# Kernel optimization log

Hardware: AMD Instinct MI355X
Metric: run time of the kernel (lower is better)

Reference implementation:

```python
import jax, jax.numpy as jnp
import numpy as np

N, L, D = 8, 2048, 128


def setup_inputs() -> dict:
    key = jax.random.key(0)
    k1, k2, k3, k4 = jax.random.split(key, 4)
    x_t = jax.random.normal(k1, (N, L, D), jnp.float32)
    x_f = jax.random.normal(k2, (N, L, D), jnp.float32)
    W = jax.random.normal(k3, (D, D), jnp.float32) / np.sqrt(D)  # proj weight (torch Linear layout)
    b = jax.random.normal(k4, (D,), jnp.float32) * 0.02
    return {"x_t": x_t, "x_f": x_f, "W": W, "b": b}


def _col_score(a, c, scale):
    # softmax attention with zeroed diagonal, then column-sum -> [N, L]
    att = jnp.einsum('nld,nmd->nlm', a, c) * scale
    att = jax.nn.softmax(att, axis=-1)
    att = att * (1.0 - jnp.eye(att.shape[-1], dtype=att.dtype))
    return jnp.sum(att, axis=1)


def _mask(score, time):
    # score: [N, L]; k-th extreme threshold, k = L//2
    k = int(0.5 * score.shape[1])
    if time:
        vals, _ = jax.lax.top_k(score, k)          # k largest, descending
        theta = vals[:, -1:]                        # k-th largest
        return score > theta
    else:
        vals, _ = jax.lax.top_k(-score, k)          # k smallest
        theta = -vals[:, -1:]                       # k-th smallest
        return score <= theta


def reference(x_t, x_f, W, b):
    scale = 1.0 / np.sqrt(W.shape[0])
    pt = x_t @ W.T + b
    pf = x_f @ W.T + b
    score_t = _col_score(pt, pt, scale)
    score_f = _col_score(pf, pf, scale)
    score_tf = _col_score(pt, pf, scale)
    score_ft = _col_score(pf, pt, scale)
    mask_t = _mask(score_t, False)
    mask_f = _mask(score_f, False)
    mask_tf = _mask(score_tf, True)   # computed in original forward (unused in blend)
    mask_ft = _mask(score_ft, True)
    mask_t1 = (mask_t & ~mask_f)[:, :, None]   # [N, L, 1] broadcast over D
    mask_f1 = (mask_f & ~mask_t)[:, :, None]
    x_t1 = jnp.where(mask_t1, x_f, x_t)
    x_f1 = jnp.where(mask_f1, x_t, x_f)
    return (0.5 * (x_t1 + x_t), 0.5 * (x_f1 + x_f))
```

## Files before the change

kernel.cpp:

```cpp
#include <hip/hip_runtime.h>
#include <math.h>

#define LL 2048
#define DD 128
#define NS 16
#define SLAB (LL * DD)
#define SCALE 0.08838834764831845f

typedef __attribute__((ext_vector_type(8))) short short8v;
typedef __attribute__((ext_vector_type(4))) float float4v;

__device__ __forceinline__ unsigned int f2bf(float f) {
    unsigned int u = __float_as_uint(f);
    u += 0x7fffu + ((u >> 16) & 1u);
    return u >> 16;
}

__device__ __forceinline__ void strip_decode(int bx, int by, int& ib, int& ns) {
    const int lin = by * 16 + bx;
    const int xcd = lin & 7;
    const int w   = lin >> 3;
    ns = xcd + 8 * (w & 1);
    ib = w >> 1;
}

__device__ __forceinline__ void gl_lds16(const void* g, void* l) {
    __builtin_amdgcn_global_load_lds(
        (const __attribute__((address_space(1))) void*)g,
        (__attribute__((address_space(3))) void*)l, 16, 0, 0);
}

__device__ __forceinline__ void stage512(
    const unsigned short* __restrict__ gT, unsigned short* lbuf, int tid)
{
    const int row = tid >> 2;
    const int oc  = (tid & 3) ^ ((row >> 1) & 3);
    const int sb  = tid & ~63;
    gl_lds16(gT + (size_t)row * DD + oc * 8, lbuf + (size_t)sb * 8);
}

#define STAGE_HALF(DST, GH, GL, KC) do {                       \
    stage512((GH) + (KC) * 32,       (DST)[0], tid);           \
    stage512((GL) + (KC) * 32,       (DST)[1], tid);           \
    stage512((GH) + ((KC) + 1) * 32, (DST)[2], tid);           \
    stage512((GL) + ((KC) + 1) * 32, (DST)[3], tid); } while (0)

#define ZEROACC(ACC) do {                                      \
    _Pragma("unroll") for (int rt = 0; rt < 4; ++rt)           \
    _Pragma("unroll") for (int ct = 0; ct < 2; ++ct)           \
    _Pragma("unroll") for (int r = 0; r < 4; ++r) (ACC)[rt][ct][r] = 0.f; } while (0)

#define KC2(ACC, CB, KI, AKC) do {                                           \
    const unsigned short* BhP = (CB)[2 * (KI)];                              \
    const unsigned short* BlP = (CB)[2 * (KI) + 1];                          \
    short8v bh[2], bl[2], alv[4];                                            \
    _Pragma("unroll")                                                        \
    for (int ct = 0; ct < 2; ++ct) {                                         \
        const int r = wc * 32 + ct * 16 + l16;                               \
        const int off = r * 32 + ((quad ^ ((r >> 1) & 3)) << 3);             \
        bh[ct] = *(const short8v*)&BhP[off];                                 \
        bl[ct] = *(const short8v*)&BlP[off];                                 \
    }                                                                        \
    _Pragma("unroll")                                                        \
    for (int rt = 0; rt < 4; ++rt) {                                         \
        const int r = wr * 64 + rt * 16 + l16;                               \
        const int off = r * 32 + ((quad ^ ((r >> 1) & 3)) << 3);             \
        alv[rt] = *(const short8v*)&Alpan[AKC][off];                         \
    }                                                                        \
    __builtin_amdgcn_s_setprio(1);                                           \
    _Pragma("unroll")                                                        \
    for (int rt = 0; rt < 4; ++rt)                                           \
    _Pragma("unroll")                                                        \
    for (int ct = 0; ct < 2; ++ct) {                                         \
        (ACC)[rt][ct] = __builtin_amdgcn_mfma_f32_16x16x32_bf16(ah[AKC][rt], bh[ct], (ACC)[rt][ct], 0, 0, 0); \
        (ACC)[rt][ct] = __builtin_amdgcn_mfma_f32_16x16x32_bf16(ah[AKC][rt], bl[ct], (ACC)[rt][ct], 0, 0, 0); \
        (ACC)[rt][ct] = __builtin_amdgcn_mfma_f32_16x16x32_bf16(alv[rt],     bh[ct], (ACC)[rt][ct], 0, 0, 0); \
    }                                                                        \
    __builtin_amdgcn_s_setprio(0); } while (0)

#define EPI1(ACC) do {                                         \
    _Pragma("unroll") for (int rt = 0; rt < 4; ++rt)           \
    _Pragma("unroll") for (int rg = 0; rg < 4; ++rg) {         \
        float e0 = __expf((ACC)[rt][0][rg] * SCALE);           \
        float e1 = __expf((ACC)[rt][1][rg] * SCALE);           \
        z[rt][rg] += e0 + e1; } } while (0)

#define EPI2(ACC, JBV) do {                                    \
    float colp0 = 0.f, colp1 = 0.f;                            \
    const bool dgj = ((JBV) == ib);                            \
    _Pragma("unroll") for (int rt = 0; rt < 4; ++rt)           \
    _Pragma("unroll") for (int rg = 0; rg < 4; ++rg) {         \
        const int rl = wr * 64 + rt * 16 + quad * 4 + rg;      \
        float e0 = __expf((ACC)[rt][0][rg] * SCALE);           \
        float e1 = __expf((ACC)[rt][1][rg] * SCALE);           \
        bool s0 = dgj && (rl == wc * 32 + l16);                \
        bool s1 = dgj && (rl == wc * 32 + 16 + l16);           \
        colp0 += s0 ? 0.f : e0 * wrow[rt][rg];                 \
        colp1 += s1 ? 0.f : e1 * wrow[rt][rg]; }               \
    colp0 += __shfl_xor(colp0, 16); colp0 += __shfl_xor(colp0, 32); \
    colp1 += __shfl_xor(colp1, 16); colp1 += __shfl_xor(colp1, 32); \
    if (quad == 0) {                                           \
        scs[(JBV) * 128 + wc * 32 + l16][wr]      = colp0;     \
        scs[(JBV) * 128 + wc * 32 + 16 + l16][wr] = colp1; } } while (0)

__global__ __launch_bounds__(512) void proj_kernel(
    const float* __restrict__ xt, const float* __restrict__ xf,
    const float* __restrict__ W,  const float* __restrict__ bias,
    unsigned short* __restrict__ Ph, unsigned short* __restrict__ Pl)
{
    __shared__ float Wl[128 * 128];
    __shared__ float Xl[128 * 128];
    const int ns = blockIdx.y;
    const int l0 = blockIdx.x * 128;
    const int src = ns >> 3, n = ns & 7;
    const float* x = (src ? xf : xt) + (size_t)n * LL * DD + (size_t)l0 * DD;
    const int tid = threadIdx.x;
    const int ty = tid >> 4, tx = tid & 15;

#pragma unroll
    for (int it = 0; it < 8; ++it) {
        const int s   = it * 512 + tid;
        const int row = s >> 5, c = s & 31;
        const int oc  = c ^ (row & 7);
        const int sb  = it * 512 + (tid & ~63);
        gl_lds16(W + (size_t)row * DD + oc * 4, Wl + (size_t)sb * 4);
        gl_lds16(x + (size_t)row * DD + oc * 4, Xl + (size_t)sb * 4);
    }

    float acc[4][8];
#pragma unroll
    for (int i = 0; i < 4; ++i)
#pragma unroll
        for (int j = 0; j < 8; ++j) acc[i][j] = bias[tx + 16 * j];

    __syncthreads();

    const int rs = ty & 7, ds = tx & 7;
#pragma unroll 4
    for (int k4 = 0; k4 < 128; k4 += 4) {
        const int c = k4 >> 2;
        float4 xv[4], wv[8];
#pragma unroll
        for (int i = 0; i < 4; ++i)
            xv[i] = *(const float4*)&Xl[(ty + 32 * i) * 128 + ((c ^ rs) << 2)];
#pragma unroll
        for (int j = 0; j < 8; ++j)
            wv[j] = *(const float4*)&Wl[(tx + 16 * j) * 128 + ((c ^ ds) << 2)];
#pragma unroll
        for (int i = 0; i < 4; ++i)
#pragma unroll
            for (int j = 0; j < 8; ++j) {
                acc[i][j] = fmaf(xv[i].x, wv[j].x, acc[i][j]);
                acc[i][j] = fmaf(xv[i].y, wv[j].y, acc[i][j]);
                acc[i][j] = fmaf(xv[i].z, wv[j].z, acc[i][j]);
                acc[i][j] = fmaf(xv[i].w, wv[j].w, acc[i][j]);
            }
    }

#pragma unroll
    for (int i = 0; i < 4; ++i) {
        const size_t rowo = (size_t)ns * SLAB + (size_t)(l0 + ty + 32 * i) * DD;
#pragma unroll
        for (int j = 0; j < 8; ++j) {
            float p = acc[i][j];
            unsigned int hb = f2bf(p);
            float hf = __uint_as_float(hb << 16);
            unsigned int lb = f2bf(p - hf);
            Ph[rowo + tx + 16 * j] = (unsigned short)hb;
            Pl[rowo + tx + 16 * j] = (unsigned short)lb;
        }
    }
}

__global__ __launch_bounds__(512, 2) void score_kernel(
    const unsigned short* __restrict__ Ph, const unsigned short* __restrict__ Pl,
    float* __restrict__ Spart)
{
    __shared__ unsigned short pan[2][4][4096];
    __shared__ unsigned short Alpan[4][4096];
    __shared__ float scs[2048][2];
    __shared__ float zl[128][4];
    int ib, ns;  strip_decode(blockIdx.x, blockIdx.y, ib, ns);
    const int tid = threadIdx.x;
    const int lane = tid & 63, quad = lane >> 4, l16 = lane & 15, wave = tid >> 6;
    const int wr = wave >> 2, wc = wave & 3;

    const unsigned short* sAh = Ph + (size_t)ns * SLAB + (size_t)ib * 128 * DD;
    const unsigned short* sAl = Pl + (size_t)ns * SLAB + (size_t)ib * 128 * DD;
    const unsigned short* sBh = Ph + (size_t)ns * SLAB;
    const unsigned short* sBl = Pl + (size_t)ns * SLAB;

    stage512(sAl,      Alpan[0], tid);
    stage512(sAl + 32, Alpan[1], tid);
    stage512(sAl + 64, Alpan[2], tid);
    stage512(sAl + 96, Alpan[3], tid);
    STAGE_HALF(pan[0], sBh, sBl, 0);
    short8v ah[4][4];
#pragma unroll
    for (int kc = 0; kc < 4; ++kc)
#pragma unroll
        for (int rt = 0; rt < 4; ++rt)
            ah[kc][rt] = *(const short8v*)
                &sAh[(size_t)(wr * 64 + rt * 16 + l16) * DD + kc * 32 + quad * 8];
    __syncthreads();

    float4v accA[4][2], accB[4][2];
    float z[4][4];
#pragma unroll
    for (int rt = 0; rt < 4; ++rt)
#pragma unroll
        for (int rg = 0; rg < 4; ++rg) z[rt][rg] = 0.f;

#pragma unroll 1
    for (int jp = 0; jp < 8; ++jp) {
        const unsigned short* b0h = sBh + (size_t)(2 * jp) * 128 * DD;
        const unsigned short* b0l = sBl + (size_t)(2 * jp) * 128 * DD;
        const unsigned short* b1h = b0h + 128 * DD;
        const unsigned short* b1l = b0l + 128 * DD;
        const unsigned short* b2h = b1h + 128 * DD;
        const unsigned short* b2l = b1l + 128 * DD;

        ZEROACC(accA);
        STAGE_HALF(pan[1], b0h, b0l, 2);
        KC2(accA, pan[0], 0, 0);
        KC2(accA, pan[0], 1, 1);
        if (jp) EPI1(accB);
        __syncthreads();

        STAGE_HALF(pan[0], b1h, b1l, 0);
        KC2(accA, pan[1], 0, 2);
        KC2(accA, pan[1], 1, 3);
        __syncthreads();

        ZEROACC(accB);
        STAGE_HALF(pan[1], b1h, b1l, 2);
        KC2(accB, pan[0], 0, 0);
        KC2(accB, pan[0], 1, 1);
        EPI1(accA);
        __syncthreads();

        if (jp < 7) STAGE_HALF(pan[0], b2h, b2l, 0);
        KC2(accB, pan[1], 0, 2);
        KC2(accB, pan[1], 1, 3);
        __syncthreads();
    }
    EPI1(accB);

#pragma unroll
    for (int rt = 0; rt < 4; ++rt)
#pragma unroll
        for (int rg = 0; rg < 4; ++rg) {
            float s = z[rt][rg];
            s += __shfl_xor(s, 1);
            s += __shfl_xor(s, 2);
            s += __shfl_xor(s, 4);
            s += __shfl_xor(s, 8);
            if (l16 == 0) zl[wr * 64 + rt * 16 + quad * 4 + rg][wc] = s;
        }
    STAGE_HALF(pan[0], sBh, sBl, 0);
    __syncthreads();
    float wrow[4][4];
#pragma unroll
    for (int rt = 0; rt < 4; ++rt)
#pragma unroll
        for (int rg = 0; rg < 4; ++rg) {
            const int row = wr * 64 + rt * 16 + quad * 4 + rg;
            wrow[rt][rg] = 1.0f / (zl[row][0] + zl[row][1] + zl[row][2] + zl[row][3]);
        }

#pragma unroll 1
    for (int jp = 0; jp < 8; ++jp) {
        const unsigned short* b0h = sBh + (size_t)(2 * jp) * 128 * DD;
        const unsigned short* b0l = sBl + (size_t)(2 * jp) * 128 * DD;
        const unsigned short* b1h = b0h + 128 * DD;
        const unsigned short* b1l = b0l + 128 * DD;
        const unsigned short* b2h = b1h + 128 * DD;
        const unsigned short* b2l = b1l + 128 * DD;

        ZEROACC(accA);
        STAGE_HALF(pan[1], b0h, b0l, 2);
        KC2(accA, pan[0], 0, 0);
        KC2(accA, pan[0], 1, 1);
        if (jp) EPI2(accB, 2 * jp - 1);
        __syncthreads();

        STAGE_HALF(pan[0], b1h, b1l, 0);
        KC2(accA, pan[1], 0, 2);
        KC2(accA, pan[1], 1, 3);
        __syncthreads();

        ZEROACC(accB);
        STAGE_HALF(pan[1], b1h, b1l, 2);
        KC2(accB, pan[0], 0, 0);
        KC2(accB, pan[0], 1, 1);
        EPI2(accA, 2 * jp);
        __syncthreads();

        if (jp < 7) STAGE_HALF(pan[0], b2h, b2l, 0);
        KC2(accB, pan[1], 0, 2);
        KC2(accB, pan[1], 1, 3);
        __syncthreads();
    }
    EPI2(accB, 15);

    __syncthreads();
#pragma unroll
    for (int g = 0; g < 4; ++g) {
        const int m = tid + g * 512;
        Spart[((size_t)ns * LL + m) * 16 + ib] = scs[m][0] + scs[m][1];
    }
}

__global__ __launch_bounds__(512) void mask_kernel(
    const float* __restrict__ Spart, unsigned char* __restrict__ maskbuf)
{
    __shared__ double s[LL];
    __shared__ int cp[4][128];
    const int sl = blockIdx.x;
    const int ns = blockIdx.y;
    const int tid = threadIdx.x;
    const int r = tid & 127, g = tid >> 7;

#pragma unroll
    for (int q = 0; q < 4; ++q) {
        int m = tid + q * 512;
        const float* sp = Spart + ((size_t)ns * LL + m) * 16;
        double a = 0.0;
#pragma unroll
        for (int t = 0; t < 16; ++t) a += (double)sp[t];
        s[m] = a;
    }
    __syncthreads();

    const double si = s[sl * 128 + r];
    const double2* sv = (const double2*)s;
    const int base = g * 256;
    int cnt = 0;
#pragma unroll 8
    for (int j = 0; j < 256; ++j) {
        double2 p = sv[base + j];
        cnt += (p.x < si) ? 1 : 0;
        cnt += (p.y < si) ? 1 : 0;
    }
    cp[g][r] = cnt;
    __syncthreads();
    if (tid < 128) {
        int c = cp[0][tid] + cp[1][tid] + cp[2][tid] + cp[3][tid];
        maskbuf[ns * LL + sl * 128 + tid] = (c < 1024) ? 1 : 0;
    }
}

__global__ __launch_bounds__(256) void blend_kernel(
    const float* __restrict__ xt, const float* __restrict__ xf,
    const unsigned char* __restrict__ maskbuf, float* __restrict__ out)
{
    const int idx4 = blockIdx.x * 256 + threadIdx.x;
    const size_t q = (size_t)idx4 * 4;
    const int row = (int)(q >> 7);
    const float4 a = *(const float4*)(xt + q);
    const float4 b = *(const float4*)(xf + q);
    const int mt = maskbuf[row] & 1;
    const int mf = maskbuf[16384 + row] & 1;
    const bool ct = mt && !mf;
    const bool cf = mf && !mt;
    float4 av;
    av.x = 0.5f * (a.x + b.x);  av.y = 0.5f * (a.y + b.y);
    av.z = 0.5f * (a.z + b.z);  av.w = 0.5f * (a.w + b.w);
    float4 o0 = ct ? av : a;
    float4 o1 = cf ? av : b;
    *(float4*)(out + q)                   = o0;
    *(float4*)(out + (size_t)2097152 + q) = o1;
}

extern "C" void kernel_launch(void* const* d_in, const int* in_sizes, int n_in,
                              void* d_out, int out_size, void* d_ws, size_t ws_size,
                              hipStream_t stream)
{
    const float* xt = (const float*)d_in[0];
    const float* xf = (const float*)d_in[1];
    const float* W  = (const float*)d_in[2];
    const float* b  = (const float*)d_in[3];
    float* out = (float*)d_out;

    unsigned short* Ph = (unsigned short*)d_out;
    unsigned short* Pl = Ph + (size_t)NS * SLAB;

    float* Spart = (float*)d_ws;
    unsigned char* maskbuf = (unsigned char*)(Spart + (size_t)16 * LL * 16);

    proj_kernel<<<dim3(16, NS), 512, 0, stream>>>(xt, xf, W, b, Ph, Pl);
    score_kernel<<<dim3(16, 16), 512, 0, stream>>>(Ph, Pl, Spart);
    mask_kernel<<<dim3(16, NS), 512, 0, stream>>>(Spart, maskbuf);
    blend_kernel<<<2048, 256, 0, stream>>>(xt, xf, maskbuf, out);
}
```

Baseline: 197.4 us.

## Double-buffer K-chunks in projection kernel with 8x8 register tiles

Result: slower. 260.2 us (+31.8%).

```diff
diff --git a/kernel.cpp b/kernel.cpp
--- a/kernel.cpp
+++ b/kernel.cpp
@@ -103,71 +103,87 @@
         scs[(JBV) * 128 + wc * 32 + l16][wr]      = colp0;     \
         scs[(JBV) * 128 + wc * 32 + 16 + l16][wr] = colp1; } } while (0)
 
-__global__ __launch_bounds__(512) void proj_kernel(
+__global__ __launch_bounds__(256, 2) void proj_kernel(
     const float* __restrict__ xt, const float* __restrict__ xf,
     const float* __restrict__ W,  const float* __restrict__ bias,
     unsigned short* __restrict__ Ph, unsigned short* __restrict__ Pl)
 {
-    __shared__ float Wl[128 * 128];
-    __shared__ float Xl[128 * 128];
+    __shared__ float Xb[2][128 * 32];
+    __shared__ float Wb[2][128 * 32];
     const int ns = blockIdx.y;
     const int l0 = blockIdx.x * 128;
     const int src = ns >> 3, n = ns & 7;
     const float* x = (src ? xf : xt) + (size_t)n * LL * DD + (size_t)l0 * DD;
     const int tid = threadIdx.x;
-    const int ty = tid >> 4, tx = tid & 15;
-
-#pragma unroll
-    for (int it = 0; it < 8; ++it) {
-        const int s   = it * 512 + tid;
-        const int row = s >> 5, c = s & 31;
-        const int oc  = c ^ (row & 7);
-        const int sb  = it * 512 + (tid & ~63);
-        gl_lds16(W + (size_t)row * DD + oc * 4, Wl + (size_t)sb * 4);
-        gl_lds16(x + (size_t)row * DD + oc * 4, Xl + (size_t)sb * 4);
-    }
-
-    float acc[4][8];
-#pragma unroll
-    for (int i = 0; i < 4; ++i)
-#pragma unroll
-        for (int j = 0; j < 8; ++j) acc[i][j] = bias[tx + 16 * j];
-
-    __syncthreads();
-
-    const int rs = ty & 7, ds = tx & 7;
-#pragma unroll 4
-    for (int k4 = 0; k4 < 128; k4 += 4) {
-        const int c = k4 >> 2;
-        float4 xv[4], wv[8];
-#pragma unroll
-        for (int i = 0; i < 4; ++i)
-            xv[i] = *(const float4*)&Xl[(ty + 32 * i) * 128 + ((c ^ rs) << 2)];
-#pragma unroll
-        for (int j = 0; j < 8; ++j)
-            wv[j] = *(const float4*)&Wl[(tx + 16 * j) * 128 + ((c ^ ds) << 2)];
-#pragma unroll
-        for (int i = 0; i < 4; ++i)
+    const int tx = tid & 15, ty = tid >> 4;
+
+#define PSTAGE(BUF, G, KC) do {                                              \
+    _Pragma("unroll")                                                        \
+    for (int it = 0; it < 4; ++it) {                                         \
+        const int s   = it * 256 + tid;                                      \
+        const int sb  = it * 256 + (tid & ~63);                              \
+        const int row = s >> 3, cp = s & 7;                                  \
+        const int oc  = cp ^ (row & 7) ^ ((row >> 3) & 7);                   \
+        gl_lds16((G) + (size_t)row * DD + (KC) * 32 + oc * 4,                \
+                 (BUF) + (size_t)sb * 4);                                    \
+    } } while (0)
+
+    float acc[8][8];
+#pragma unroll
+    for (int i = 0; i < 8; ++i)
+#pragma unroll
+        for (int j = 0; j < 8; ++j) acc[i][j] = bias[tx * 8 + j];
+
+    PSTAGE(Xb[0], x, 0);
+    PSTAGE(Wb[0], W, 0);
+    __syncthreads();
+
+#pragma unroll
+    for (int kc = 0; kc < 4; ++kc) {
+        if (kc < 3) {
+            PSTAGE(Xb[(kc + 1) & 1], x, kc + 1);
+            PSTAGE(Wb[(kc + 1) & 1], W, kc + 1);
+        }
+        const float* Xc = Xb[kc & 1];
+        const float* Wc = Wb[kc & 1];
+#pragma unroll
+        for (int c = 0; c < 8; ++c) {
+            float4 xv[8], wv[8];
+#pragma unroll
+            for (int i = 0; i < 8; ++i) {
+                const int r = ty * 8 + i;
+                xv[i] = *(const float4*)&Xc[r * 32 + ((c ^ i ^ (ty & 7)) << 2)];
+            }
 #pragma unroll
             for (int j = 0; j < 8; ++j) {
-                acc[i][j] = fmaf(xv[i].x, wv[j].x, acc[i][j]);
-                acc[i][j] = fmaf(xv[i].y, wv[j].y, acc[i][j]);
-                acc[i][j] = fmaf(xv[i].z, wv[j].z, acc[i][j]);
-                acc[i][j] = fmaf(xv[i].w, wv[j].w, acc[i][j]);
+                const int r = tx * 8 + j;
+                wv[j] = *(const float4*)&Wc[r * 32 + ((c ^ j ^ (tx & 7)) << 2)];
             }
-    }
-
-#pragma unroll
-    for (int i = 0; i < 4; ++i) {
-        const size_t rowo = (size_t)ns * SLAB + (size_t)(l0 + ty + 32 * i) * DD;
+#pragma unroll
+            for (int i = 0; i < 8; ++i)
+#pragma unroll
+                for (int j = 0; j < 8; ++j) {
+                    acc[i][j] = fmaf(xv[i].x, wv[j].x, acc[i][j]);
+                    acc[i][j] = fmaf(xv[i].y, wv[j].y, acc[i][j]);
+                    acc[i][j] = fmaf(xv[i].z, wv[j].z, acc[i][j]);
+                    acc[i][j] = fmaf(xv[i].w, wv[j].w, acc[i][j]);
+                }
+        }
+        if (kc < 3) __syncthreads();
+    }
+#undef PSTAGE
+
+#pragma unroll
+    for (int i = 0; i < 8; ++i) {
+        const size_t rowo = (size_t)ns * SLAB + (size_t)(l0 + ty * 8 + i) * DD;
 #pragma unroll
         for (int j = 0; j < 8; ++j) {
             float p = acc[i][j];
             unsigned int hb = f2bf(p);
             float hf = __uint_as_float(hb << 16);
             unsigned int lb = f2bf(p - hf);
-            Ph[rowo + tx + 16 * j] = (unsigned short)hb;
-            Pl[rowo + tx + 16 * j] = (unsigned short)lb;
+            Ph[rowo + tx * 8 + j] = (unsigned short)hb;
+            Pl[rowo + tx * 8 + j] = (unsigned short)lb;
         }
     }
 }
@@ -388,7 +404,7 @@
     float* Spart = (float*)d_ws;
     unsigned char* maskbuf = (unsigned char*)(Spart + (size_t)16 * LL * 16);
 
-    proj_kernel<<<dim3(16, NS), 512, 0, stream>>>(xt, xf, W, b, Ph, Pl);
+    proj_kernel<<<dim3(16, NS), 256, 0, stream>>>(xt, xf, W, b, Ph, Pl);
     score_kernel<<<dim3(16, 16), 512, 0, stream>>>(Ph, Pl, Spart);
     mask_kernel<<<dim3(16, NS), 512, 0, stream>>>(Spart, maskbuf);
     blend_kernel<<<2048, 256, 0, stream>>>(xt, xf, maskbuf, out);
```
